# Kernel optimization log

Hardware: AMD Instinct MI355X
Metric: run time of the kernel (lower is better)

## Reference

```python
import jax, jax.numpy as jnp
import numpy as np

NU = 200000  # user nodes
NI = 200000  # item nodes
N = NU + NI  # union node space: users [0,NU), items [NU,N)
D = 64
K = 2        # TAGConv hops
E = 1000000  # edges per relation
EPS = 1e-5


def _tagconv(x, src, dst, W, b):
    # DGL TAGConv over homogeneous (union) graph: norm = in_deg.clamp(min=1)^-0.5,
    # each hop: h = norm * (A @ (norm * h)); linear over concat of k+1 hop features.
    deg = jax.ops.segment_sum(jnp.ones(src.shape[0], x.dtype), dst, num_segments=N)
    norm = jnp.maximum(deg, 1.0) ** -0.5
    hs = [x]
    h = x
    for _ in range(K):
        h = h * norm[:, None]
        h = jax.ops.segment_sum(h[src], dst, num_segments=N)  # SpMM scatter-add
        h = h * norm[:, None]
        hs.append(h)
    return jnp.concatenate(hs, axis=-1) @ W + b


def _bn_silu(x, g, b):
    # BatchNorm1d (training-mode batch stats) + SiLU; dropout is identity (eval)
    mu = jnp.mean(x, axis=0)
    var = jnp.var(x, axis=0)
    y = (x - mu) * jax.lax.rsqrt(var + EPS) * g + b
    return y * jax.nn.sigmoid(y)


def setup_inputs() -> dict:
    key = jax.random.key(0)
    ks = jax.random.split(key, 12)
    inp = {
        'user_emb': jax.random.normal(ks[0], (NU, D), jnp.float32),
        'item_emb': jax.random.normal(ks[1], (NI, D), jnp.float32),
        'W_go1': jax.random.normal(ks[2], ((K + 1) * D, D), jnp.float32) * 0.05,
        'b_go1': jnp.zeros((D,), jnp.float32),
        'W_back1': jax.random.normal(ks[3], ((K + 1) * D, D), jnp.float32) * 0.05,
        'b_back1': jnp.zeros((D,), jnp.float32),
        'W_go2': jax.random.normal(ks[4], ((K + 1) * D, D), jnp.float32) * 0.05,
        'b_go2': jnp.zeros((D,), jnp.float32),
        'W_back2': jax.random.normal(ks[5], ((K + 1) * D, D), jnp.float32) * 0.05,
        'b_back2': jnp.zeros((D,), jnp.float32),
        'g1u': jnp.ones((D,), jnp.float32), 'be1u': jnp.zeros((D,), jnp.float32),
        'g1i': jnp.ones((D,), jnp.float32), 'be1i': jnp.zeros((D,), jnp.float32),
        'g2u': jnp.ones((D,), jnp.float32), 'be2u': jnp.zeros((D,), jnp.float32),
        'g2i': jnp.ones((D,), jnp.float32), 'be2i': jnp.zeros((D,), jnp.float32),
        'go_src': jax.random.randint(ks[6], (E,), 0, NU, jnp.int64),
        'go_dst': jax.random.randint(ks[7], (E,), 0, NI, jnp.int64),
        'back_src': jax.random.randint(ks[8], (E,), 0, NI, jnp.int64),
        'back_dst': jax.random.randint(ks[9], (E,), 0, NU, jnp.int64),
    }
    return inp


def reference(user_emb, item_emb, W_go1, b_go1, W_back1, b_back1,
              W_go2, b_go2, W_back2, b_back2,
              g1u, be1u, g1i, be1i, g2u, be2u, g2i, be2i,
              go_src, go_dst, back_src, back_dst):
    # union-index edge lists: go = user->item, back = item->user
    gs, gd = go_src, go_dst + NU
    bs, bd = back_src + NU, back_dst

    x = jnp.concatenate([user_emb, item_emb], axis=0)  # [N, D]
    # layer 1: each dst type receives from exactly one relation -> mean is identity
    h_item = _tagconv(x, gs, gd, W_go1, b_go1)[NU:]
    h_user = _tagconv(x, bs, bd, W_back1, b_back1)[:NU]
    h_user = _bn_silu(h_user, g1u, be1u)
    h_item = _bn_silu(h_item, g1i, be1i)

    x2 = jnp.concatenate([h_user, h_item], axis=0)
    h_item2 = _tagconv(x2, gs, gd, W_go2, b_go2)[NU:]
    h_user2 = _tagconv(x2, bs, bd, W_back2, b_back2)[:NU]
    h_user2 = _bn_silu(h_user2, g2u, be2u)
    h_item2 = _bn_silu(h_item2, g2i, be2i)

    return jnp.concatenate([h_user2, h_item2], axis=0)  # [N, out2]
```

## Files before the change

kernel.cpp:

```cpp
#include <hip/hip_runtime.h>
#include <cstdint>
#include <cstddef>

#define RN 200000
#define NR2 400000
#define DIM 64
#define NE 1000000
#define NB_PR 391
#define NBB 782
#define ET 4096
#define NBLK 489
#define NBLKP 512

typedef __attribute__((ext_vector_type(8))) short short8v;
typedef __attribute__((ext_vector_type(4))) float f32x4;
typedef __attribute__((ext_vector_type(8))) unsigned short us8;
typedef __attribute__((ext_vector_type(2))) unsigned int uint2v;

struct Ptrs16 { const void* p[16]; };

struct GemmCfg {
  const unsigned short* Agg;
  const unsigned short* Xd;
  const unsigned short* Wp;
  const float* bias;
  unsigned short* Hout;
  float* stats;
};

__device__ __forceinline__ float bf2f(unsigned short u){
  unsigned int x = ((unsigned int)u) << 16;
  return __builtin_bit_cast(float, x);
}
__device__ __forceinline__ unsigned short f2bf(float f){
  unsigned int x = __builtin_bit_cast(unsigned int, f);
  unsigned int r = x + 0x7fffu + ((x >> 16) & 1u);
  return (unsigned short)(r >> 16);
}

__global__ __launch_bounds__(256) void detect2_k(const unsigned short* emb,
                                                 const unsigned int* esrc,
                                                 int* flags, Ptrs16 ps,
                                                 float* params, float* stats){
  __shared__ int cnt0, cnt1, sf0;
  int t = threadIdx.x;
  if (t == 0){ cnt0 = 0; cnt1 = 0; }
  __syncthreads();
  int c0 = 0, c1 = 0;
  #pragma unroll
  for (int s = 0; s < 4; ++s){
    int i = (t*4 + s) * 14;
    float af = fabsf(bf2f(emb[i]));
    if (af > 0.0009765625f && af < 32.0f) c0++;
    int e = t*4 + s;
    if (esrc[2*e + 1] != 0u) c1++;
  }
  atomicAdd(&cnt0, c0); atomicAdd(&cnt1, c1);
  __syncthreads();
  if (t == 0){
    int f0 = (cnt0 > 512) ? 1 : 0;
    int f1 = (cnt1 < 512) ? 1 : 0;
    flags[0] = f0; flags[1] = f1; sf0 = f0;
  }
  __syncthreads();
  int f0 = sf0;
  const int aidx[12] = {1,3,5,7,8,9,10,11,12,13,14,15};
  const int aoff[12] = {12288,24640,36992,49344,49408,49472,49536,49600,49664,49728,49792,49856};
  for (int base = t; base < 768; base += 256){
    int a = base >> 6, j = base & 63;
    const void* p = ps.p[aidx[a]];
    params[aoff[a] + j] = f0 ? bf2f(((const unsigned short*)p)[j]) : ((const float*)p)[j];
  }
  for (int z = t; z < 512; z += 256) stats[z] = 0.0f;
}

__global__ __launch_bounds__(256) void convpp_k(const void* uin, const void* iin,
                                                unsigned short* __restrict__ out,
                                                Ptrs16 ps, unsigned short* __restrict__ wpack,
                                                const int* flags, int n8){
  int bid = blockIdx.x;
  if (bid < 128){
    int i = bid*256 + threadIdx.x;
    int m = i >> 13, f = i & 8191;
    int r   = f & 7;
    int c16 = (f >> 3) & 15;
    int kg  = (f >> 7) & 3;
    int c   = (f >> 9) & 3;
    int t2  = (f >> 11) & 1;
    int s   = (f >> 12) & 1;
    int k = s*64 + t2*32 + kg*8 + r;
    int j = k*DIM + c*16 + c16;
    const void* wp = ps.p[m*2];
    float v = flags[0] ? bf2f(((const unsigned short*)wp)[j]) : ((const float*)wp)[j];
    wpack[i] = f2bf(v);
    return;
  }
  int i = (bid - 128)*256 + threadIdx.x;
  if (i >= n8) return;
  int item = (i >= RN*8);
  const void* in = item ? iin : uin;
  int li = item ? i - RN*8 : i;
  us8 o;
  if (flags[0]){
    o = ((const us8*)in)[li];
  } else {
    const float* f = (const float*)in + (size_t)li*8;
    #pragma unroll
    for (int r = 0; r < 8; ++r) o[r] = f2bf(f[r]);
  }
  ((us8*)out)[i] = o;
}

__global__ __launch_bounds__(256) void pass12_k(const unsigned int* go_src, const unsigned int* go_dst,
                                                const unsigned int* back_src, const unsigned int* back_dst,
                                                int* __restrict__ C, int* __restrict__ Rloc,
                                                unsigned int* __restrict__ slab, const int* flags){
  __shared__ unsigned int spk[ET];
  __shared__ unsigned short sbk[ET];
  __shared__ int h[1024];
  __shared__ int ps[256];
  int blk = blockIdx.x, t = threadIdx.x;
  #pragma unroll
  for (int q = 0; q < 4; ++q) h[t + q*256] = 0;
  __syncthreads();
  int i64 = flags[1];
  int e0 = blk*ET;
  #pragma unroll
  for (int j = 0; j < 16; ++j){
    int e = e0 + j*256 + t;
    int li = j*256 + t;
    if (e < 2*NE){
      int rel = e >= NE;
      int ei = rel ? e - NE : e;
      const unsigned int* pd = rel ? back_dst : go_dst;
      const unsigned int* psr = rel ? back_src : go_src;
      int d  = i64 ? (int)pd[2*ei]  : (int)pd[ei];
      int sc = i64 ? (int)psr[2*ei] : (int)psr[ei];
      int b = (rel ? NB_PR : 0) + (d >> 9);
      spk[li] = (unsigned)sc | ((unsigned)(d & 511) << 18);
      sbk[li] = (unsigned short)b;
      atomicAdd(&h[b], 1);
    } else {
      sbk[li] = 0xFFFFu;
    }
  }
  __syncthreads();
  int c4[4], p4[4]; int s = 0;
  #pragma unroll
  for (int q = 0; q < 4; ++q){ c4[q] = h[t*4 + q]; p4[q] = s; s += c4[q]; }
  ps[t] = s;
  __syncthreads();
  for (int o = 1; o < 256; o <<= 1){
    int x = (t >= o) ? ps[t-o] : 0;
    __syncthreads();
    ps[t] += x;
    __syncthreads();
  }
  int base = (t > 0) ? ps[t-1] : 0;
  #pragma unroll
  for (int q = 0; q < 4; ++q){
    int b = t*4 + q;
    if (b < NBB){
      C[b*NBLKP + blk]    = c4[q];
      Rloc[b*NBLKP + blk] = base + p4[q];
    }
  }
  __syncthreads();
  #pragma unroll
  for (int q = 0; q < 4; ++q){
    int b = t*4 + q;
    h[b] = base + p4[q];
  }
  __syncthreads();
  #pragma unroll
  for (int j = 0; j < 16; ++j){
    int li = j*256 + t;
    unsigned short b = sbk[li];
    if (b != 0xFFFFu){
      int pos = atomicAdd(&h[b], 1);
      slab[(size_t)blk*ET + pos] = spk[li];
    }
  }
}

__global__ __launch_bounds__(256) void sizes_k(const int* __restrict__ C, int* __restrict__ S){
  int w = blockIdx.x*4 + (threadIdx.x >> 6);
  int lane = threadIdx.x & 63;
  if (w >= NBB) return;
  int sum = 0;
  for (int k = lane; k < NBLK; k += 64) sum += C[w*NBLKP + k];
  #pragma unroll
  for (int o = 32; o > 0; o >>= 1) sum += __shfl_down(sum, o, 64);
  if (lane == 0) S[w] = sum;
}

__global__ __launch_bounds__(1024) void scanS_k(const int* __restrict__ S, int* __restrict__ s0,
                                                int* __restrict__ rs){
  __shared__ int sh[1024];
  int t = threadIdx.x;
  int v = (t < NBB) ? S[t] : 0;
  sh[t] = v;
  __syncthreads();
  for (int o = 1; o < 1024; o <<= 1){
    int x = (t >= o) ? sh[t-o] : 0;
    __syncthreads();
    sh[t] += x;
    __syncthreads();
  }
  if (t < NBB) s0[t] = sh[t] - v;
  if (t == NBB-1){ s0[NBB] = sh[t]; rs[NR2] = 2*NE; }
}

__global__ __launch_bounds__(512) void buildCSR3_k(const int* __restrict__ C,
                                                   const int* __restrict__ Rloc,
                                                   const int* __restrict__ s0g,
                                                   const unsigned int* __restrict__ slab,
                                                   int* __restrict__ rs, int* __restrict__ col){
  __shared__ int lcnt[512], lsc[512], lcur[512];
  int b = blockIdx.x, t = threadIdx.x;
  int cnt = 0, rst = 0;
  if (t < NBLK){ cnt = C[b*NBLKP + t]; rst = Rloc[b*NBLKP + t]; }
  lcnt[t] = 0;
  __syncthreads();
  const unsigned int* sl = slab + (size_t)t*ET + rst;
  for (int k = 0; k < cnt; ++k){
    unsigned int q = sl[k];
    atomicAdd(&lcnt[q >> 18], 1);
  }
  __syncthreads();
  int rv = lcnt[t];
  lsc[t] = rv;
  __syncthreads();
  for (int o = 1; o < 512; o <<= 1){
    int x = (t >= o) ? lsc[t-o] : 0;
    __syncthreads();
    lsc[t] += x;
    __syncthreads();
  }
  int s0b = s0g[b];
  int d0 = (b < NB_PR) ? b*512 : RN + (b - NB_PR)*512;
  int relEnd = (b < NB_PR) ? RN : NR2;
  int rows = relEnd - d0; if (rows > 512) rows = 512;
  int srcoff = (b < NB_PR) ? 0 : RN;
  int start = lsc[t] - rv;
  lcur[t] = start;
  if (t < rows) rs[d0 + t] = s0b + start;
  __syncthreads();
  for (int k = 0; k < cnt; ++k){
    unsigned int q = sl[k];
    int p = atomicAdd(&lcur[q >> 18], 1);
    col[s0b + p] = (int)(q & 0x3FFFFu) + srcoff;
  }
}

__global__ __launch_bounds__(256) void spmmU_k(const int* __restrict__ rs, const int* __restrict__ col,
                                               const unsigned short* __restrict__ Xg,
                                               unsigned short* outA, unsigned short* outB){
  int wv = (int)((blockIdx.x*256 + threadIdx.x) >> 6);
  int lane = threadIdx.x & 63;
  int el = lane & 7;
  int eb = lane & 56;
  int row = wv*8 + (lane >> 3);
  int b = rs[row], e = rs[row+1];
  int deg = e - b;
  int md = deg;
  #pragma unroll
  for (int o = 8; o < 64; o <<= 1) md = max(md, __shfl_xor(md, o, 64));
  float ac[8];
  #pragma unroll
  for (int r = 0; r < 8; ++r) ac[r] = 0.0f;

  if (md <= 8){
    if (md > 0){
      int cv = col[b + ((el < deg) ? el : 0)];
      us8 v[8];
      #pragma unroll
      for (int j = 0; j < 8; ++j){
        int ix = __shfl(cv, eb + j, 64);
        ix = ((unsigned)ix < (unsigned)NR2) ? ix : 0;
        v[j] = *(const us8*)((const char*)Xg + (((size_t)(unsigned)ix) << 7) + (el << 4));
      }
      #pragma unroll
      for (int j = 0; j < 8; ++j){
        if (j < deg){
          #pragma unroll
          for (int r = 0; r < 8; ++r) ac[r] += bf2f(v[j][r]);
        }
      }
    }
  } else {
    for (int i = 0; i < md; i += 16){
      int o0 = i + el, o1 = i + 8 + el;
      int cv0 = col[b + ((o0 < deg) ? o0 : 0)];
      int cv1 = col[b + ((o1 < deg) ? o1 : 0)];
      us8 v[16];
      #pragma unroll
      for (int j = 0; j < 8; ++j){
        int ix = __shfl(cv0, eb + j, 64);
        ix = ((unsigned)ix < (unsigned)NR2) ? ix : 0;
        v[j] = *(const us8*)((const char*)Xg + (((size_t)(unsigned)ix) << 7) + (el << 4));
      }
      #pragma unroll
      for (int j = 0; j < 8; ++j){
        int ix = __shfl(cv1, eb + j, 64);
        ix = ((unsigned)ix < (unsigned)NR2) ? ix : 0;
        v[8+j] = *(const us8*)((const char*)Xg + (((size_t)(unsigned)ix) << 7) + (el << 4));
      }
      #pragma unroll
      for (int j = 0; j < 16; ++j){
        if (i + j < deg){
          #pragma unroll
          for (int r = 0; r < 8; ++r) ac[r] += bf2f(v[j][r]);
        }
      }
    }
  }
  float nrm = deg > 0 ? rsqrtf((float)deg) : 1.0f;
  us8 pv;
  #pragma unroll
  for (int r = 0; r < 8; ++r) pv[r] = f2bf(ac[r]*nrm);
  unsigned short* ob = (row < RN) ? (outA + ((size_t)row << 6))
                                  : (outB + ((size_t)(row - RN) << 6));
  __builtin_nontemporal_store(pv, (us8*)ob + el);
}

__global__ __launch_bounds__(256) void gemm2m_k(GemmCfg cA, GemmCfg cB){
  __shared__ float ls[128];
  __shared__ unsigned short stg[4][16][72];
  for (int t0 = threadIdx.x; t0 < 128; t0 += 256) ls[t0] = 0.0f;
  __syncthreads();
  int half = (int)(gridDim.x >> 1);
  bool sec = ((int)blockIdx.x >= half);
  const unsigned short* Agg = sec ? cB.Agg : cA.Agg;
  const unsigned short* Xd  = sec ? cB.Xd  : cA.Xd;
  const unsigned short* Wp  = sec ? cB.Wp  : cA.Wp;
  const float* bias         = sec ? cB.bias : cA.bias;
  unsigned short* Hout      = sec ? cB.Hout : cA.Hout;
  float* stats              = sec ? cB.stats : cA.stats;
  int lb = sec ? (int)blockIdx.x - half : (int)blockIdx.x;
  int lane = threadIdx.x & 63;
  int w = (int)(threadIdx.x >> 6);
  int gw = lb*4 + w;
  int nw = half*4;
  int c16 = lane & 15, kg = lane >> 4;

  short8v Bf[2][2][4];
  #pragma unroll
  for (int s = 0; s < 2; ++s)
    #pragma unroll
    for (int t2 = 0; t2 < 2; ++t2)
      #pragma unroll
      for (int c = 0; c < 4; ++c)
        Bf[s][t2][c] = ((const short8v*)Wp)[(((s*2 + t2)*4 + c)*4 + kg)*16 + c16];
  float bc[4];
  #pragma unroll
  for (int c = 0; c < 4; ++c) bc[c] = bias[c*16 + c16];

  const short8v* xd = (const short8v*)Xd;
  const short8v* ag = (const short8v*)Agg;
  const int npair = RN/32;
  float ssum[4] = {0,0,0,0}, ssq[4] = {0,0,0,0};

  short8v cur[8], nxt[8];
  int tp = gw;
  if (tp < npair){
    size_t ra = (size_t)(tp*32 + c16);
    size_t rb = ra + 16;
    cur[0] = xd[ra*8 + kg];     cur[1] = xd[ra*8 + 4 + kg];
    cur[2] = ag[ra*8 + kg];     cur[3] = ag[ra*8 + 4 + kg];
    cur[4] = xd[rb*8 + kg];     cur[5] = xd[rb*8 + 4 + kg];
    cur[6] = ag[rb*8 + kg];     cur[7] = ag[rb*8 + 4 + kg];
  }
  for (; tp < npair; ){
    int tn = tp + nw;
    if (tn < npair){
      size_t ra = (size_t)(tn*32 + c16);
      size_t rb = ra + 16;
      nxt[0] = xd[ra*8 + kg];   nxt[1] = xd[ra*8 + 4 + kg];
      nxt[2] = ag[ra*8 + kg];   nxt[3] = ag[ra*8 + 4 + kg];
      nxt[4] = xd[rb*8 + kg];   nxt[5] = xd[rb*8 + 4 + kg];
      nxt[6] = ag[rb*8 + kg];   nxt[7] = ag[rb*8 + 4 + kg];
    }
    #pragma unroll
    for (int h = 0; h < 2; ++h){
      f32x4 acc4[4];
      #pragma unroll
      for (int c = 0; c < 4; ++c){ f32x4 z = {bc[c],bc[c],bc[c],bc[c]}; acc4[c] = z; }
      #pragma unroll
      for (int c = 0; c < 4; ++c){
        acc4[c] = __builtin_amdgcn_mfma_f32_16x16x32_bf16(cur[h*4+0], Bf[0][0][c], acc4[c], 0, 0, 0);
        acc4[c] = __builtin_amdgcn_mfma_f32_16x16x32_bf16(cur[h*4+1], Bf[0][1][c], acc4[c], 0, 0, 0);
        acc4[c] = __builtin_amdgcn_mfma_f32_16x16x32_bf16(cur[h*4+2], Bf[1][0][c], acc4[c], 0, 0, 0);
        acc4[c] = __builtin_amdgcn_mfma_f32_16x16x32_bf16(cur[h*4+3], Bf[1][1][c], acc4[c], 0, 0, 0);
      }
      #pragma unroll
      for (int c = 0; c < 4; ++c)
        #pragma unroll
        for (int r = 0; r < 4; ++r){
          float v = acc4[c][r];
          ssum[c] += v; ssq[c] += v*v;
          stg[w][kg*4 + r][c*16 + c16] = f2bf(v);
        }
      size_t rb0 = (size_t)(tp*32 + h*16);
      #pragma unroll
      for (int q = 0; q < 2; ++q){
        int li = q*64 + lane;
        int rr = li >> 3;
        int cc = (li & 7) << 3;
        us8 ov = *(const us8*)&stg[w][rr][cc];
        __builtin_nontemporal_store(ov, (us8*)(Hout + (rb0 + rr)*DIM + cc));
      }
    }
    #pragma unroll
    for (int q = 0; q < 8; ++q) cur[q] = nxt[q];
    tp = tn;
  }
  #pragma unroll
  for (int c = 0; c < 4; ++c){
    atomicAdd(&ls[c*16 + c16], ssum[c]);
    atomicAdd(&ls[64 + c*16 + c16], ssq[c]);
  }
  __syncthreads();
  for (int t0 = threadIdx.x; t0 < 128; t0 += 256) atomicAdd(&stats[t0], ls[t0]);
}

__global__ __launch_bounds__(256) void bnapply2_k(unsigned short* H,
                                                  const float* __restrict__ stats,
                                                  const float* __restrict__ gI, const float* __restrict__ beI,
                                                  const float* __restrict__ gU, const float* __restrict__ beU,
                                                  int n8){
  __shared__ float lac[256];
  int t = threadIdx.x;
  if (t < 128){
    int usr = (t < 64);
    int j = t & 63;
    const float* st = usr ? stats + 128 : stats;
    float mu  = st[j]    * (1.0f/RN);
    float var = st[64+j] * (1.0f/RN) - mu*mu;
    float inv = rsqrtf(var + 1e-5f);
    float g  = usr ? gU[j]  : gI[j];
    float be = usr ? beU[j] : beI[j];
    float a = g * inv;
    int o = usr ? 0 : 128;
    lac[o + j] = a;
    lac[o + 64 + j] = be - mu*a;
  }
  __syncthreads();
  int i = blockIdx.x*256 + t;
  if (i >= n8) return;
  const float* ac = (i < RN*8) ? lac : lac + 128;
  us8 v = ((us8*)H)[i];
  int cb = (i*8) & 63;
  #pragma unroll
  for (int r = 0; r < 8; ++r){
    float x = bf2f(v[r]);
    float y = ac[cb+r]*x + ac[64+cb+r];
    float o = y / (1.0f + expf(-y));
    v[r] = f2bf(o);
  }
  ((us8*)H)[i] = v;
}

__global__ __launch_bounds__(256) void bnout2_k(const unsigned short* __restrict__ Hu,
                                                const unsigned short* __restrict__ Hi,
                                                const float* __restrict__ stats,
                                                const float* __restrict__ gI, const float* __restrict__ beI,
                                                const float* __restrict__ gU, const float* __restrict__ beU,
                                                void* out, const int* __restrict__ flags, int n8){
  __shared__ float lac[256];
  int t = threadIdx.x;
  if (t < 128){
    int usr = (t < 64);
    int j = t & 63;
    const float* st = usr ? stats + 128 : stats;
    float mu  = st[j]    * (1.0f/RN);
    float var = st[64+j] * (1.0f/RN) - mu*mu;
    float inv = rsqrtf(var + 1e-5f);
    float g  = usr ? gU[j]  : gI[j];
    float be = usr ? beU[j] : beI[j];
    float a = g * inv;
    int o = usr ? 0 : 128;
    lac[o + j] = a;
    lac[o + 64 + j] = be - mu*a;
  }
  __syncthreads();
  int i = blockIdx.x*256 + t;
  if (i >= n8) return;
  int item = (i >= RN*8);
  const float* ac = item ? lac + 128 : lac;
  us8 v = item ? ((const us8*)Hi)[i - RN*8] : ((const us8*)Hu)[i];
  int cb = (i*8) & 63;
  float o[8];
  #pragma unroll
  for (int r = 0; r < 8; ++r){
    float x = bf2f(v[r]);
    float y = ac[cb+r]*x + ac[64+cb+r];
    o[r] = y / (1.0f + expf(-y));
  }
  if (flags[0]){
    unsigned short* ob = (unsigned short*)out + (size_t)i*8;
    us8 wv;
    #pragma unroll
    for (int r = 0; r < 8; ++r) wv[r] = f2bf(o[r]);
    __builtin_nontemporal_store(wv, (us8*)ob);
  } else {
    float* ob = (float*)out + (size_t)i*8;
    f32x4 w0 = {o[0],o[1],o[2],o[3]}, w1 = {o[4],o[5],o[6],o[7]};
    __builtin_nontemporal_store(w0, (f32x4*)ob);
    __builtin_nontemporal_store(w1, (f32x4*)ob + 1);
  }
}

extern "C" void kernel_launch(void* const* d_in, const int* in_sizes, int n_in,
                              void* d_out, int out_size, void* d_ws, size_t ws_size,
                              hipStream_t stream){
  (void)in_sizes; (void)n_in; (void)out_size;
  const void* user_emb = d_in[0];
  const void* item_emb = d_in[1];
  const void* go_src   = d_in[18];
  const void* go_dst   = d_in[19];
  const void* back_src = d_in[20];
  const void* back_dst = d_in[21];

  char* ws = (char*)d_ws;
  size_t off = 0;
  auto alloc = [&](size_t bytes) -> void* {
    void* p = ws + off;
    off += (bytes + 255) & ~((size_t)255);
    return p;
  };
  int*   flags  = (int*)  alloc(64);
  float* params = (float*)alloc((size_t)49920*4);
  unsigned short* wpack = (unsigned short*)alloc((size_t)4*8192*2);
  float* stats  = (float*)alloc(512*4);
  int*   Cmat   = (int*)  alloc((size_t)NBB*NBLKP*4);
  int*   Rloc   = (int*)  alloc((size_t)NBB*NBLKP*4);
  int*   Sbuf   = (int*)  alloc(1024*4);
  int*   s0g    = (int*)  alloc(1024*4);
  int*   rs_all = (int*)  alloc((size_t)(NR2+1)*4);
  int*   col_all= (int*)  alloc(((size_t)2*NE + 64)*4);
  unsigned short* x1   = (unsigned short*)alloc((size_t)NR2*DIM*2);
  unsigned short* x2   = (unsigned short*)alloc((size_t)NR2*DIM*2);
  unsigned short* agg1 = (unsigned short*)alloc((size_t)RN*DIM*2);
  if (off > ws_size) return;

  unsigned int* slab = (unsigned int*)x2;

  unsigned short* x1u = x1;
  unsigned short* x1i = x1 + (size_t)RN*DIM;
  unsigned short* x2u = x2;
  unsigned short* x2i = x2 + (size_t)RN*DIM;

  const int G8A = (NR2*DIM/8)/256;
  const int GSU = NR2/32;

  float* b_go1 = params + 12288;
  float* b_bk1 = params + 24640;
  float* b_go2 = params + 36992;
  float* b_bk2 = params + 49344;
  float* g1u = params + 49408; float* be1u = params + 49472;
  float* g1i = params + 49536; float* be1i = params + 49600;
  float* g2u = params + 49664; float* be2u = params + 49728;
  float* g2i = params + 49792; float* be2i = params + 49856;

  Ptrs16 ps;
  for (int i = 0; i < 16; ++i) ps.p[i] = d_in[2+i];

  detect2_k<<<1,256,0,stream>>>((const unsigned short*)user_emb, (const unsigned int*)go_src,
                                flags, ps, params, stats);
  convpp_k<<<G8A + 128,256,0,stream>>>(user_emb, item_emb, x1, ps, wpack, flags, NR2*DIM/8);

  pass12_k<<<NBLK,256,0,stream>>>((const unsigned int*)go_src, (const unsigned int*)go_dst,
                                  (const unsigned int*)back_src, (const unsigned int*)back_dst,
                                  Cmat, Rloc, slab, flags);
  sizes_k<<<(NBB+3)/4,256,0,stream>>>(Cmat, Sbuf);
  scanS_k<<<1,1024,0,stream>>>(Sbuf, s0g, rs_all);
  buildCSR3_k<<<NBB,512,0,stream>>>(Cmat, Rloc, s0g, slab, rs_all, col_all);

  spmmU_k<<<GSU,256,0,stream>>>(rs_all, col_all, x1, agg1, x2u);
  {
    GemmCfg go1{agg1, x1i, wpack + 0*8192, b_go1, x2i, stats + 0};
    GemmCfg bk1{x2u,  x1u, wpack + 1*8192, b_bk1, x2u, stats + 128};
    gemm2m_k<<<1024,256,0,stream>>>(go1, bk1);
  }
  bnapply2_k<<<G8A,256,0,stream>>>(x2, stats, g1i, be1i, g1u, be1u, NR2*DIM/8);

  spmmU_k<<<GSU,256,0,stream>>>(rs_all, col_all, x2, x1u, x1i);
  {
    GemmCfg go2{x1u, x2i, wpack + 2*8192, b_go2, agg1, stats + 256};
    GemmCfg bk2{x1i, x2u, wpack + 3*8192, b_bk2, x1i,  stats + 384};
    gemm2m_k<<<1024,256,0,stream>>>(go2, bk2);
  }
  bnout2_k<<<G8A,256,0,stream>>>(x1i, agg1, stats + 256, g2i, be2i, g2u, be2u,
                                 d_out, flags, NR2*DIM/8);
}
```

Measured before the change: 322.7 us.

## Fuse sparse aggregation with the per-relation GEMM and BN statistics kernel

Replaces the separate SpMM kernel and the persistent GEMM kernel with one kernel per layer. Each block aggregates 32 rows into shared memory, then runs the MFMA GEMM against the dense self features directly from LDS and writes the output plus BatchNorm partial sums. This removes the global write and re-read of the aggregated intermediate and one launch per layer. In exchange, the GEMM loses its persistent prefetch loop and weight reuse across tiles. Each of the much larger number of blocks now issues its own global atomics for the statistics, which adds contention.

```diff
diff --git a/kernel.cpp b/kernel.cpp
--- a/kernel.cpp
+++ b/kernel.cpp
@@ -15,12 +15,10 @@
 typedef __attribute__((ext_vector_type(8))) short short8v;
 typedef __attribute__((ext_vector_type(4))) float f32x4;
 typedef __attribute__((ext_vector_type(8))) unsigned short us8;
-typedef __attribute__((ext_vector_type(2))) unsigned int uint2v;
 
 struct Ptrs16 { const void* p[16]; };
 
 struct GemmCfg {
-  const unsigned short* Agg;
   const unsigned short* Xd;
   const unsigned short* Wp;
   const float* bias;
@@ -253,175 +251,141 @@
   }
 }
 
-__global__ __launch_bounds__(256) void spmmU_k(const int* __restrict__ rs, const int* __restrict__ col,
+__global__ __launch_bounds__(256) void fused_k(const int* __restrict__ rs,
+                                               const int* __restrict__ col,
                                                const unsigned short* __restrict__ Xg,
-                                               unsigned short* outA, unsigned short* outB){
-  int wv = (int)((blockIdx.x*256 + threadIdx.x) >> 6);
-  int lane = threadIdx.x & 63;
-  int el = lane & 7;
-  int eb = lane & 56;
-  int row = wv*8 + (lane >> 3);
-  int b = rs[row], e = rs[row+1];
-  int deg = e - b;
-  int md = deg;
-  #pragma unroll
-  for (int o = 8; o < 64; o <<= 1) md = max(md, __shfl_xor(md, o, 64));
-  float ac[8];
-  #pragma unroll
-  for (int r = 0; r < 8; ++r) ac[r] = 0.0f;
-
-  if (md <= 8){
-    if (md > 0){
-      int cv = col[b + ((el < deg) ? el : 0)];
-      us8 v[8];
-      #pragma unroll
-      for (int j = 0; j < 8; ++j){
-        int ix = __shfl(cv, eb + j, 64);
-        ix = ((unsigned)ix < (unsigned)NR2) ? ix : 0;
-        v[j] = *(const us8*)((const char*)Xg + (((size_t)(unsigned)ix) << 7) + (el << 4));
+                                               GemmCfg cA, GemmCfg cB){
+  __shared__ unsigned short stg[32][72];
+  __shared__ unsigned short ostg[2][16][72];
+  __shared__ float ls[128];
+  int t = threadIdx.x;
+  for (int i = t; i < 128; i += 256) ls[i] = 0.0f;
+  int r0 = (int)blockIdx.x * 32;
+  bool rel = (r0 >= RN);
+  const unsigned short* Xd = rel ? cB.Xd : cA.Xd;
+  const unsigned short* Wp = rel ? cB.Wp : cA.Wp;
+  const float* bias        = rel ? cB.bias : cA.bias;
+  unsigned short* Hout     = rel ? cB.Hout : cA.Hout;
+  float* stats             = rel ? cB.stats : cA.stats;
+  int lr0 = rel ? r0 - RN : r0;
+
+  int lane = t & 63;
+  int w = t >> 6;
+  {
+    int el = lane & 7, eb = lane & 56;
+    int lr = w*8 + (lane >> 3);
+    int row = r0 + lr;
+    int b = rs[row], e = rs[row+1];
+    int deg = e - b;
+    int md = deg;
+    #pragma unroll
+    for (int o = 8; o < 64; o <<= 1) md = max(md, __shfl_xor(md, o, 64));
+    float ac[8];
+    #pragma unroll
+    for (int r = 0; r < 8; ++r) ac[r] = 0.0f;
+    if (md <= 8){
+      if (md > 0){
+        int cv = col[b + ((el < deg) ? el : 0)];
+        us8 v[8];
+        #pragma unroll
+        for (int j = 0; j < 8; ++j){
+          int ix = __shfl(cv, eb + j, 64);
+          ix = ((unsigned)ix < (unsigned)NR2) ? ix : 0;
+          v[j] = *(const us8*)((const char*)Xg + (((size_t)(unsigned)ix) << 7) + (el << 4));
+        }
+        #pragma unroll
+        for (int j = 0; j < 8; ++j){
+          if (j < deg){
+            #pragma unroll
+            for (int r = 0; r < 8; ++r) ac[r] += bf2f(v[j][r]);
+          }
+        }
       }
-      #pragma unroll
-      for (int j = 0; j < 8; ++j){
-        if (j < deg){
-          #pragma unroll
-          for (int r = 0; r < 8; ++r) ac[r] += bf2f(v[j][r]);
+    } else {
+      for (int i = 0; i < md; i += 16){
+        int o0 = i + el, o1 = i + 8 + el;
+        int cv0 = col[b + ((o0 < deg) ? o0 : 0)];
+        int cv1 = col[b + ((o1 < deg) ? o1 : 0)];
+        us8 v[16];
+        #pragma unroll
+        for (int j = 0; j < 8; ++j){
+          int ix = __shfl(cv0, eb + j, 64);
+          ix = ((unsigned)ix < (unsigned)NR2) ? ix : 0;
+          v[j] = *(const us8*)((const char*)Xg + (((size_t)(unsigned)ix) << 7) + (el << 4));
+        }
+        #pragma unroll
+        for (int j = 0; j < 8; ++j){
+          int ix = __shfl(cv1, eb + j, 64);
+          ix = ((unsigned)ix < (unsigned)NR2) ? ix : 0;
+          v[8+j] = *(const us8*)((const char*)Xg + (((size_t)(unsigned)ix) << 7) + (el << 4));
+        }
+        #pragma unroll
+        for (int j = 0; j < 16; ++j){
+          if (i + j < deg){
+            #pragma unroll
+            for (int r = 0; r < 8; ++r) ac[r] += bf2f(v[j][r]);
+          }
         }
       }
     }
-  } else {
-    for (int i = 0; i < md; i += 16){
-      int o0 = i + el, o1 = i + 8 + el;
-      int cv0 = col[b + ((o0 < deg) ? o0 : 0)];
-      int cv1 = col[b + ((o1 < deg) ? o1 : 0)];
-      us8 v[16];
-      #pragma unroll
-      for (int j = 0; j < 8; ++j){
-        int ix = __shfl(cv0, eb + j, 64);
-        ix = ((unsigned)ix < (unsigned)NR2) ? ix : 0;
-        v[j] = *(const us8*)((const char*)Xg + (((size_t)(unsigned)ix) << 7) + (el << 4));
-      }
-      #pragma unroll
-      for (int j = 0; j < 8; ++j){
-        int ix = __shfl(cv1, eb + j, 64);
-        ix = ((unsigned)ix < (unsigned)NR2) ? ix : 0;
-        v[8+j] = *(const us8*)((const char*)Xg + (((size_t)(unsigned)ix) << 7) + (el << 4));
-      }
-      #pragma unroll
-      for (int j = 0; j < 16; ++j){
-        if (i + j < deg){
-          #pragma unroll
-          for (int r = 0; r < 8; ++r) ac[r] += bf2f(v[j][r]);
-        }
-      }
-    }
-  }
-  float nrm = deg > 0 ? rsqrtf((float)deg) : 1.0f;
-  us8 pv;
-  #pragma unroll
-  for (int r = 0; r < 8; ++r) pv[r] = f2bf(ac[r]*nrm);
-  unsigned short* ob = (row < RN) ? (outA + ((size_t)row << 6))
-                                  : (outB + ((size_t)(row - RN) << 6));
-  __builtin_nontemporal_store(pv, (us8*)ob + el);
-}
-
-__global__ __launch_bounds__(256) void gemm2m_k(GemmCfg cA, GemmCfg cB){
-  __shared__ float ls[128];
-  __shared__ unsigned short stg[4][16][72];
-  for (int t0 = threadIdx.x; t0 < 128; t0 += 256) ls[t0] = 0.0f;
-  __syncthreads();
-  int half = (int)(gridDim.x >> 1);
-  bool sec = ((int)blockIdx.x >= half);
-  const unsigned short* Agg = sec ? cB.Agg : cA.Agg;
-  const unsigned short* Xd  = sec ? cB.Xd  : cA.Xd;
-  const unsigned short* Wp  = sec ? cB.Wp  : cA.Wp;
-  const float* bias         = sec ? cB.bias : cA.bias;
-  unsigned short* Hout      = sec ? cB.Hout : cA.Hout;
-  float* stats              = sec ? cB.stats : cA.stats;
-  int lb = sec ? (int)blockIdx.x - half : (int)blockIdx.x;
-  int lane = threadIdx.x & 63;
-  int w = (int)(threadIdx.x >> 6);
-  int gw = lb*4 + w;
-  int nw = half*4;
+    float nrm = deg > 0 ? rsqrtf((float)deg) : 1.0f;
+    us8 pv;
+    #pragma unroll
+    for (int r = 0; r < 8; ++r) pv[r] = f2bf(ac[r]*nrm);
+    *(us8*)&stg[lr][el*8] = pv;
+  }
+  __syncthreads();
+  int h = w >> 1, cp = w & 1;
   int c16 = lane & 15, kg = lane >> 4;
-
-  short8v Bf[2][2][4];
+  short8v Bf[2][2][2];
   #pragma unroll
   for (int s = 0; s < 2; ++s)
     #pragma unroll
     for (int t2 = 0; t2 < 2; ++t2)
       #pragma unroll
-      for (int c = 0; c < 4; ++c)
-        Bf[s][t2][c] = ((const short8v*)Wp)[(((s*2 + t2)*4 + c)*4 + kg)*16 + c16];
-  float bc[4];
-  #pragma unroll
-  for (int c = 0; c < 4; ++c) bc[c] = bias[c*16 + c16];
+      for (int cc = 0; cc < 2; ++cc)
+        Bf[s][t2][cc] = ((const short8v*)Wp)[(((s*2 + t2)*4 + (cp*2 + cc))*4 + kg)*16 + c16];
+  float bc[2];
+  #pragma unroll
+  for (int cc = 0; cc < 2; ++cc) bc[cc] = bias[(cp*2 + cc)*16 + c16];
 
   const short8v* xd = (const short8v*)Xd;
-  const short8v* ag = (const short8v*)Agg;
-  const int npair = RN/32;
-  float ssum[4] = {0,0,0,0}, ssq[4] = {0,0,0,0};
-
-  short8v cur[8], nxt[8];
-  int tp = gw;
-  if (tp < npair){
-    size_t ra = (size_t)(tp*32 + c16);
-    size_t rb = ra + 16;
-    cur[0] = xd[ra*8 + kg];     cur[1] = xd[ra*8 + 4 + kg];
-    cur[2] = ag[ra*8 + kg];     cur[3] = ag[ra*8 + 4 + kg];
-    cur[4] = xd[rb*8 + kg];     cur[5] = xd[rb*8 + 4 + kg];
-    cur[6] = ag[rb*8 + kg];     cur[7] = ag[rb*8 + 4 + kg];
-  }
-  for (; tp < npair; ){
-    int tn = tp + nw;
-    if (tn < npair){
-      size_t ra = (size_t)(tn*32 + c16);
-      size_t rb = ra + 16;
-      nxt[0] = xd[ra*8 + kg];   nxt[1] = xd[ra*8 + 4 + kg];
-      nxt[2] = ag[ra*8 + kg];   nxt[3] = ag[ra*8 + 4 + kg];
-      nxt[4] = xd[rb*8 + kg];   nxt[5] = xd[rb*8 + 4 + kg];
-      nxt[6] = ag[rb*8 + kg];   nxt[7] = ag[rb*8 + 4 + kg];
+  size_t gr = (size_t)(lr0 + h*16 + c16);
+  short8v A00 = xd[gr*8 + kg];
+  short8v A01 = xd[gr*8 + 4 + kg];
+  short8v A10 = *(const short8v*)&stg[h*16 + c16][kg*8];
+  short8v A11 = *(const short8v*)&stg[h*16 + c16][32 + kg*8];
+  f32x4 acc4[2];
+  #pragma unroll
+  for (int cc = 0; cc < 2; ++cc){ f32x4 z = {bc[cc],bc[cc],bc[cc],bc[cc]}; acc4[cc] = z; }
+  #pragma unroll
+  for (int cc = 0; cc < 2; ++cc){
+    acc4[cc] = __builtin_amdgcn_mfma_f32_16x16x32_bf16(A00, Bf[0][0][cc], acc4[cc], 0, 0, 0);
+    acc4[cc] = __builtin_amdgcn_mfma_f32_16x16x32_bf16(A01, Bf[0][1][cc], acc4[cc], 0, 0, 0);
+    acc4[cc] = __builtin_amdgcn_mfma_f32_16x16x32_bf16(A10, Bf[1][0][cc], acc4[cc], 0, 0, 0);
+    acc4[cc] = __builtin_amdgcn_mfma_f32_16x16x32_bf16(A11, Bf[1][1][cc], acc4[cc], 0, 0, 0);
+  }
+  #pragma unroll
+  for (int cc = 0; cc < 2; ++cc){
+    float ssum = 0.0f, ssq = 0.0f;
+    #pragma unroll
+    for (int r = 0; r < 4; ++r){
+      float v = acc4[cc][r];
+      ssum += v; ssq += v*v;
+      ostg[h][kg*4 + r][cp*32 + cc*16 + c16] = f2bf(v);
     }
-    #pragma unroll
-    for (int h = 0; h < 2; ++h){
-      f32x4 acc4[4];
-      #pragma unroll
-      for (int c = 0; c < 4; ++c){ f32x4 z = {bc[c],bc[c],bc[c],bc[c]}; acc4[c] = z; }
-      #pragma unroll
-      for (int c = 0; c < 4; ++c){
-        acc4[c] = __builtin_amdgcn_mfma_f32_16x16x32_bf16(cur[h*4+0], Bf[0][0][c], acc4[c], 0, 0, 0);
-        acc4[c] = __builtin_amdgcn_mfma_f32_16x16x32_bf16(cur[h*4+1], Bf[0][1][c], acc4[c], 0, 0, 0);
-        acc4[c] = __builtin_amdgcn_mfma_f32_16x16x32_bf16(cur[h*4+2], Bf[1][0][c], acc4[c], 0, 0, 0);
-        acc4[c] = __builtin_amdgcn_mfma_f32_16x16x32_bf16(cur[h*4+3], Bf[1][1][c], acc4[c], 0, 0, 0);
-      }
-      #pragma unroll
-      for (int c = 0; c < 4; ++c)
-        #pragma unroll
-        for (int r = 0; r < 4; ++r){
-          float v = acc4[c][r];
-          ssum[c] += v; ssq[c] += v*v;
-          stg[w][kg*4 + r][c*16 + c16] = f2bf(v);
-        }
-      size_t rb0 = (size_t)(tp*32 + h*16);
-      #pragma unroll
-      for (int q = 0; q < 2; ++q){
-        int li = q*64 + lane;
-        int rr = li >> 3;
-        int cc = (li & 7) << 3;
-        us8 ov = *(const us8*)&stg[w][rr][cc];
-        __builtin_nontemporal_store(ov, (us8*)(Hout + (rb0 + rr)*DIM + cc));
-      }
-    }
-    #pragma unroll
-    for (int q = 0; q < 8; ++q) cur[q] = nxt[q];
-    tp = tn;
-  }
-  #pragma unroll
-  for (int c = 0; c < 4; ++c){
-    atomicAdd(&ls[c*16 + c16], ssum[c]);
-    atomicAdd(&ls[64 + c*16 + c16], ssq[c]);
-  }
-  __syncthreads();
-  for (int t0 = threadIdx.x; t0 < 128; t0 += 256) atomicAdd(&stats[t0], ls[t0]);
+    atomicAdd(&ls[cp*32 + cc*16 + c16], ssum);
+    atomicAdd(&ls[64 + cp*32 + cc*16 + c16], ssq);
+  }
+  __syncthreads();
+  {
+    int rr = cp*8 + (lane >> 3);
+    int cc2 = (lane & 7) << 3;
+    us8 ov = *(const us8*)&ostg[h][rr][cc2];
+    size_t orow = (size_t)(lr0 + h*16 + rr);
+    __builtin_nontemporal_store(ov, (us8*)(Hout + orow*DIM + cc2));
+  }
+  for (int i = t; i < 128; i += 256) atomicAdd(&stats[i], ls[i]);
 }
 
 __global__ __launch_bounds__(256) void bnapply2_k(unsigned short* H,
@@ -552,7 +516,7 @@
   unsigned short* x2i = x2 + (size_t)RN*DIM;
 
   const int G8A = (NR2*DIM/8)/256;
-  const int GSU = NR2/32;
+  const int GF  = NR2/32;
 
   float* b_go1 = params + 12288;
   float* b_bk1 = params + 24640;
@@ -577,20 +541,18 @@
   scanS_k<<<1,1024,0,stream>>>(Sbuf, s0g, rs_all);
   buildCSR3_k<<<NBB,512,0,stream>>>(Cmat, Rloc, s0g, slab, rs_all, col_all);
 
-  spmmU_k<<<GSU,256,0,stream>>>(rs_all, col_all, x1, agg1, x2u);
   {
-    GemmCfg go1{agg1, x1i, wpack + 0*8192, b_go1, x2i, stats + 0};
-    GemmCfg bk1{x2u,  x1u, wpack + 1*8192, b_bk1, x2u, stats + 128};
-    gemm2m_k<<<1024,256,0,stream>>>(go1, bk1);
+    GemmCfg go1{x1i, wpack + 0*8192, b_go1, x2i, stats + 0};
+    GemmCfg bk1{x1u, wpack + 1*8192, b_bk1, x2u, stats + 128};
+    fused_k<<<GF,256,0,stream>>>(rs_all, col_all, x1, go1, bk1);
   }
   bnapply2_k<<<G8A,256,0,stream>>>(x2, stats, g1i, be1i, g1u, be1u, NR2*DIM/8);
 
-  spmmU_k<<<GSU,256,0,stream>>>(rs_all, col_all, x2, x1u, x1i);
   {
-    GemmCfg go2{x1u, x2i, wpack + 2*8192, b_go2, agg1, stats + 256};
-    GemmCfg bk2{x1i, x2u, wpack + 3*8192, b_bk2, x1i,  stats + 384};
-    gemm2m_k<<<1024,256,0,stream>>>(go2, bk2);
-  }
-  bnout2_k<<<G8A,256,0,stream>>>(x1i, agg1, stats + 256, g2i, be2i, g2u, be2u,
+    GemmCfg go2{x2i, wpack + 2*8192, b_go2, agg1, stats + 256};
+    GemmCfg bk2{x2u, wpack + 3*8192, b_bk2, x1u,  stats + 384};
+    fused_k<<<GF,256,0,stream>>>(rs_all, col_all, x2, go2, bk2);
+  }
+  bnout2_k<<<G8A,256,0,stream>>>(x1u, agg1, stats + 256, g2i, be2i, g2u, be2u,
                                  d_out, flags, NR2*DIM/8);
 }
```

Result: slower. 666.8 us (+106.7%).
